# Kernel tuning notes

Measured on AMD Instinct MI355X. Metric: run time of the kernel, lower is better.

## Reference

```python
import jax, jax.numpy as jnp
import numpy as np
from jax import lax

N, IN_DIM, OUT_DIM, E, K = 100000, 128, 128, 600000, 3

def _xavier(key, shape):
    fan_out, fan_in = shape[0], shape[1]
    limit = float(np.sqrt(6.0 / (fan_in + fan_out)))
    return jax.random.uniform(key, shape, jnp.float32, -limit, limit)

def setup_inputs() -> dict:
    key = jax.random.key(0)
    ks = jax.random.split(key, 8)
    x = jax.random.normal(ks[0], (N, IN_DIM), jnp.float32)
    edge_index0 = jax.random.randint(ks[1], (2, E), 0, N, jnp.int64)
    edge_index1 = jax.random.randint(ks[2], (2, E), 0, N, jnp.int64)
    # relation Linear weights, torch layout [out_dim, in_dim]
    W_rel = jnp.stack([_xavier(ks[3], (OUT_DIM, IN_DIM)), _xavier(ks[4], (OUT_DIM, IN_DIM))])
    W_self = _xavier(ks[5], (OUT_DIM, IN_DIM))
    # Conv1d weight [out_ch, in_ch, k], bias [out_ch]
    fan = OUT_DIM * K
    conv_w = jax.random.uniform(ks[6], (OUT_DIM, OUT_DIM, K), jnp.float32, -1.0/np.sqrt(fan), 1.0/np.sqrt(fan))
    conv_b = jax.random.uniform(ks[7], (OUT_DIM,), jnp.float32, -1.0/np.sqrt(fan), 1.0/np.sqrt(fan))
    return {"x": x, "edge_index0": edge_index0, "edge_index1": edge_index1,
            "W_rel": W_rel, "W_self": W_self, "conv_w": conv_w, "conv_b": conv_b}

def reference(x, edge_index0, edge_index1, W_rel, W_self, conv_w, conv_b):
    num_nodes = x.shape[0]
    agg = jnp.zeros((num_nodes, W_rel.shape[1]), x.dtype)
    # per-relation: gather source feats -> linear -> scatter_add into target rows
    for ei, W in ((edge_index0, W_rel[0]), (edge_index1, W_rel[1])):
        src, tgt = ei[0], ei[1]
        messages = x[src] @ W.T                      # [E, out_dim]
        agg = agg.at[tgt].add(messages)
    # self loop
    agg = agg + x @ W_self.T
    # temporal Conv1d over node axis: [1, out_dim, N], kernel 3, padding 1, + ReLU
    # (Dropout is identity in eval mode)
    y = lax.conv_general_dilated(agg.T[None], conv_w, window_strides=(1,),
                                 padding=[(1, 1)],
                                 dimension_numbers=("NCH", "OIH", "NCH"))
    y = jax.nn.relu(y + conv_b[None, :, None])
    return y[0].T                                    # [N, out_dim]
```

## Files before the change

### kernel.cpp

```cpp
#include <hip/hip_runtime.h>
#include <hip/hip_bf16.h>

typedef __hip_bfloat16 bf16;
typedef short v8s __attribute__((ext_vector_type(8)));
typedef float v4f __attribute__((ext_vector_type(4)));
typedef unsigned int u32;

#define BFLO(u) __uint_as_float((u) << 16)
#define BFHI(u) __uint_as_float((u) & 0xffff0000u)

#define CH 4096
#define MAXNB 800

__device__ __forceinline__ int block_stride(const int* e0, int E, int* sm) {
    int t = threadIdx.x;
    if (t == 0) *sm = 0;
    __syncthreads();
    int nz = 0;
    for (int i = t; i < 2048; i += 256) {
        int slot = 2 * i + 1;
        if (slot < 2 * E) nz |= (e0[slot] != 0);
    }
    if (nz) atomicOr(sm, 1);
    __syncthreads();
    return *sm ? 1 : 2;
}


__global__ __launch_bounds__(256) void front_kernel(const float4* __restrict__ x4,
                                                    uint2* __restrict__ Ab,
                                                    const float* __restrict__ Wrel,
                                                    const float* __restrict__ Wself,
                                                    const float* __restrict__ convw,
                                                    const float* __restrict__ convb,
                                                    bf16* __restrict__ B1T,
                                                    bf16* __restrict__ B2T,
                                                    float* __restrict__ cbf,
                                                    const int* __restrict__ e0,
                                                    const int* __restrict__ e1,
                                                    int* __restrict__ gcnt,
                                                    int N, int E, int nbrr,
                                                    int cvtBlocks, int prepBlocks) {
    int b = blockIdx.x;
    if (b < cvtBlocks) {
        int i = b * 256 + threadIdx.x;
        if (i >= N * 32) return;
        int n = i >> 5, g = i & 31;
        float4 f = x4[i];
        union { uint2 u; bf16 h[4]; } o;
        o.h[0] = __float2bfloat16(f.x); o.h[1] = __float2bfloat16(f.y);
        o.h[2] = __float2bfloat16(f.z); o.h[3] = __float2bfloat16(f.w);
        Ab[(size_t)n * 96 + 64 + g] = o.u;
    } else if (b < cvtBlocks + prepBlocks) {
        int i = (b - cvtBlocks) * 256 + threadIdx.x;
        if (i < 49152) {
            int co = i / 384, k = i % 384;
            float v;
            if (k < 128)      v = Wrel[co * 128 + k];
            else if (k < 256) v = Wrel[16384 + co * 128 + (k - 128)];
            else              v = Wself[co * 128 + (k - 256)];
            B1T[i] = __float2bfloat16(v);
        } else if (i < 98304) {
            int j = i - 49152;
            int co = j / 384, k = j % 384, kk = k >> 7, ci = k & 127;
            B2T[j] = __float2bfloat16(convw[co * 384 + ci * 3 + kk]);
        } else if (i < 98432) {
            int c = i - 98304;
            cbf[c] = convb[c];
        }
    } else {
        __shared__ int hist[MAXNB];
        __shared__ int smf;
        int st = block_stride(e0, E, &smf);
        int NB = 2 * nbrr;
        int t = threadIdx.x;
        for (int i = t; i < NB; i += 256) hist[i] = 0;
        __syncthreads();
        long base = (long)(b - cvtBlocks - prepBlocks) * CH;
#pragma unroll
        for (int j = 0; j < CH / 256; ++j) {
            long e = base + j * 256 + t;
            if (e < 2 * (long)E) {
                int r = e >= E;
                long idx = r ? e - E : e;
                int tgt = (r ? e1 : e0)[(size_t)(E + idx) * st];
                atomicAdd(&hist[r * nbrr + (tgt >> 8)], 1);
            }
        }
        __syncthreads();
        for (int i = t; i < NB; i += 256) if (hist[i]) atomicAdd(&gcnt[i], hist[i]);
    }
}


__global__ __launch_bounds__(256) void bscan_kernel(const int* __restrict__ gcnt,
                                                    int* __restrict__ gbase,
                                                    int* __restrict__ gcur, int NB) {
    __shared__ int tsum[256];
    int t = threadIdx.x;
    int v[4]; int s = 0;
#pragma unroll
    for (int j = 0; j < 4; ++j) { int i = t * 4 + j; v[j] = (i < NB) ? gcnt[i] : 0; s += v[j]; }
    tsum[t] = s; __syncthreads();
    for (int d = 1; d < 256; d <<= 1) {
        int add = (t >= d) ? tsum[t - d] : 0;
        __syncthreads(); tsum[t] += add; __syncthreads();
    }
    int run = tsum[t] - s;
#pragma unroll
    for (int j = 0; j < 4; ++j) {
        int i = t * 4 + j;
        if (i < NB) { gbase[i] = run; gcur[i] = run; }
        run += v[j];
    }
    if (t == 255) gbase[NB] = run;
}


__global__ __launch_bounds__(256) void dist_kernel(const int* __restrict__ e0,
                                                   const int* __restrict__ e1,
                                                   int* __restrict__ gcur,
                                                   unsigned int* __restrict__ esorted,
                                                   int E, int nbrr) {
    __shared__ int hist[MAXNB], lstart[MAXNB], lcur[MAXNB], runbase[MAXNB];
    __shared__ unsigned int ordered[CH];
    __shared__ int tsum[256];
    __shared__ int smf;
    int st = block_stride(e0, E, &smf);
    int NB = 2 * nbrr;
    int t = threadIdx.x;
    for (int i = t; i < NB; i += 256) { hist[i] = 0; lcur[i] = 0; }
    __syncthreads();
    long base = (long)blockIdx.x * CH;
    unsigned int rec[CH / 256]; short bk[CH / 256];
#pragma unroll
    for (int j = 0; j < CH / 256; ++j) {
        long e = base + j * 256 + t;
        if (e < 2 * (long)E) {
            int r = e >= E;
            long idx = r ? e - E : e;
            const int* ei = r ? e1 : e0;
            int src = ei[(size_t)idx * st];
            int tgt = ei[(size_t)(E + idx) * st];
            bk[j] = (short)(r * nbrr + (tgt >> 8));
            rec[j] = (unsigned int)src | ((unsigned int)(tgt & 255) << 17);
            atomicAdd(&hist[bk[j]], 1);
        } else bk[j] = -1;
    }
    __syncthreads();
    {
        int vv[4]; int s = 0;
#pragma unroll
        for (int j = 0; j < 4; ++j) { int i = t * 4 + j; vv[j] = (i < NB) ? hist[i] : 0; s += vv[j]; }
        tsum[t] = s; __syncthreads();
        for (int d = 1; d < 256; d <<= 1) {
            int add = (t >= d) ? tsum[t - d] : 0;
            __syncthreads(); tsum[t] += add; __syncthreads();
        }
        int run = tsum[t] - s;
#pragma unroll
        for (int j = 0; j < 4; ++j) { int i = t * 4 + j; if (i < NB) { lstart[i] = run; run += vv[j]; } }
    }
    __syncthreads();
    for (int i = t; i < NB; i += 256) if (hist[i]) runbase[i] = atomicAdd(&gcur[i], hist[i]);
    __syncthreads();
#pragma unroll
    for (int j = 0; j < CH / 256; ++j) if (bk[j] >= 0) {
        int p = lstart[bk[j]] + atomicAdd(&lcur[bk[j]], 1);
        ordered[p] = rec[j];
    }
    __syncthreads();
    int w = t >> 6, lane = t & 63;
    for (int b = w; b < NB; b += 4) {
        int n = hist[b];
        if (n) {
            int gp = runbase[b], lp = lstart[b];
            for (int q = lane; q < n; q += 64) esorted[gp + q] = ordered[lp + q];
        }
    }
}


__global__ __launch_bounds__(256) void csr_kernel(const unsigned int* __restrict__ esorted,
                                                  const int* __restrict__ gbase,
                                                  int* __restrict__ off, int* __restrict__ cnt,
                                                  int* __restrict__ esrc, int N, int nbrr) {
    __shared__ int hist[256], lcur[256], tsum[256];
    int b = blockIdx.x;
    int r = b >= nbrr;
    int g = r ? b - nbrr : b;
    int t = threadIdx.x;
    int s0 = gbase[b], s1 = gbase[b + 1];
    hist[t] = 0;
    __syncthreads();
    for (int i = s0 + t; i < s1; i += 256)
        atomicAdd(&hist[(esorted[i] >> 17) & 255], 1);
    __syncthreads();
    int h = hist[t];
    tsum[t] = h; __syncthreads();
    for (int d = 1; d < 256; d <<= 1) {
        int add = (t >= d) ? tsum[t - d] : 0;
        __syncthreads(); tsum[t] += add; __syncthreads();
    }
    int start = tsum[t] - h;
    int node = g * 256 + t;
    if (node < N) { off[r * N + node] = s0 + start; cnt[r * N + node] = h; }
    lcur[t] = start;
    __syncthreads();
    for (int i = s0 + t; i < s1; i += 256) {
        unsigned int rec = esorted[i];
        int tl = (rec >> 17) & 255;
        int p = atomicAdd(&lcur[tl], 1);
        esrc[s0 + p] = rec & 0x1FFFF;
    }
}

__global__ __launch_bounds__(256) void gather_kernel(const int* __restrict__ off,
                                                     const int* __restrict__ cnt,
                                                     const int* __restrict__ esrc,
                                                     uint4* __restrict__ Ab4, int N) {
    int grp = blockIdx.x * 16 + (threadIdx.x >> 4);
    int lane = threadIdx.x & 15;
    if (grp >= 2 * N) return;
    int r = (grp >= N);
    int n = r ? grp - N : grp;
    int s0 = off[grp], c = cnt[grp];
    float a0 = 0.f, a1 = 0.f, a2 = 0.f, a3 = 0.f, a4 = 0.f, a5 = 0.f, a6 = 0.f, a7 = 0.f;
    for (int i0 = 0; i0 < c; i0 += 8) {
        int cm1 = c - 1;
        int s[8]; uint4 v[8];
#pragma unroll
        for (int u = 0; u < 8; ++u) {
            int j = i0 + u; j = (j <= cm1) ? j : cm1;
            s[u] = esrc[s0 + j];
        }
#pragma unroll
        for (int u = 0; u < 8; ++u)
            v[u] = Ab4[(size_t)s[u] * 48 + 32 + lane];
#pragma unroll
        for (int u = 0; u < 8; ++u) {
            if (i0 + u < c) {
                a0 += BFLO(v[u].x); a1 += BFHI(v[u].x);
                a2 += BFLO(v[u].y); a3 += BFHI(v[u].y);
                a4 += BFLO(v[u].z); a5 += BFHI(v[u].z);
                a6 += BFLO(v[u].w); a7 += BFHI(v[u].w);
            }
        }
    }
    union { uint4 u; bf16 h[8]; } o;
    o.h[0] = __float2bfloat16(a0); o.h[1] = __float2bfloat16(a1);
    o.h[2] = __float2bfloat16(a2); o.h[3] = __float2bfloat16(a3);
    o.h[4] = __float2bfloat16(a4); o.h[5] = __float2bfloat16(a5);
    o.h[6] = __float2bfloat16(a6); o.h[7] = __float2bfloat16(a7);
    Ab4[(size_t)n * 48 + (size_t)r * 16 + lane] = o.u;
}


__device__ __forceinline__ void gl2lds16(const void* g, void* l) {
    __builtin_amdgcn_global_load_lds(
        (const __attribute__((address_space(1))) u32*)g,
        (__attribute__((address_space(3))) u32*)l, 16, 0, 0);
}

__global__ __launch_bounds__(256) void gemm12_kernel(const bf16* __restrict__ Ab,
                                                     const bf16* __restrict__ B1T,
                                                     const bf16* __restrict__ B2T,
                                                     const float* __restrict__ cbf,
                                                     float* __restrict__ out, int M) {
    __shared__ __align__(16) char ldsbuf[52016];
    bf16* agg = (bf16*)ldsbuf;
    char* Ast = ldsbuf;
    char* Bst = ldsbuf + 35632;

    int t = threadIdx.x;
    int lane = t & 63, wv = t >> 6;
    int r = lane & 15, qq = lane >> 4;
    int m0 = blockIdx.x * 128;
    int swz = (r & 7) << 4;
    int lsw = ((lane & 7) ^ (lane >> 3)) << 4;

    int rowLo = (m0 < 8) ? 8 - m0 : 0;
    int rowHi = (m0 + 136 > M) ? M - m0 + 8 : 144;
    bool bdry = (rowLo > 0) || (rowHi < 144);

    const char* AbB = (const char*)Ab;
    const char* B1B = (const char*)B1T;
    const char* B2B = (const char*)B2T;

    v4f acc[9][2] = {};
    for (int kt = 0; kt < 6; ++kt) {
        int k0b = kt * 128;
        for (int c = wv; c < 34; c += 4) {
            if (c < 18) {
                int ar = m0 - 8 + c * 8 + (lane >> 3);
                ar = ar < 0 ? 0 : (ar >= M ? M - 1 : ar);
                gl2lds16(AbB + (size_t)ar * 768 + k0b + lsw, Ast + c * 1024);
            } else {
                int row = (c - 18) * 8 + (lane >> 3);
                gl2lds16(B1B + (size_t)row * 768 + k0b + lsw, Bst + (c - 18) * 1024);
            }
        }
        __syncthreads();
        if (bdry) {
            int* A4 = (int*)Ast;
            for (int i = t; i < rowLo * 32; i += 256) A4[i] = 0;
            for (int i = t; i < (144 - rowHi) * 32; i += 256) A4[rowHi * 32 + i] = 0;
            __syncthreads();
        }
#pragma unroll
        for (int ks = 0; ks < 2; ++ks) {
            int cb = (ks * 64 + qq * 16) ^ swz;
            v8s bfr[2];
#pragma unroll
            for (int tn = 0; tn < 2; ++tn)
                bfr[tn] = *(const v8s*)(Bst + (wv * 32 + tn * 16 + r) * 128 + cb);
#pragma unroll
            for (int tm = 0; tm < 9; ++tm) {
                v8s af = *(const v8s*)(Ast + (tm * 16 + r) * 128 + cb);
#pragma unroll
                for (int tn = 0; tn < 2; ++tn)
                    acc[tm][tn] = __builtin_amdgcn_mfma_f32_16x16x32_bf16(af, bfr[tn], acc[tm][tn], 0, 0, 0);
            }
        }
        __syncthreads();
    }
#pragma unroll
    for (int tm = 0; tm < 9; ++tm)
#pragma unroll
        for (int tn = 0; tn < 2; ++tn)
#pragma unroll
            for (int reg = 0; reg < 4; ++reg) {
                int row = tm * 16 + qq * 4 + reg;
                if (row >= 7 && row < 138)
                    agg[(row - 7) * 136 + wv * 32 + tn * 16 + r] =
                        __float2bfloat16(acc[tm][tn][reg]);
            }
    __syncthreads();

    v4f acc2[8][2] = {};
    for (int kt = 0; kt < 6; ++kt) {
        int k0b = kt * 128;
        int kk = kt >> 1;
        int rem = (kt & 1) * 64;
        for (int c = wv; c < 16; c += 4)
            gl2lds16(B2B + (size_t)(c * 8 + (lane >> 3)) * 768 + k0b + lsw, Bst + c * 1024);
        __syncthreads();
#pragma unroll
        for (int ks = 0; ks < 2; ++ks) {
            int cb = (ks * 64 + qq * 16) ^ swz;
            v8s bfr[2];
#pragma unroll
            for (int tn = 0; tn < 2; ++tn)
                bfr[tn] = *(const v8s*)(Bst + (wv * 32 + tn * 16 + r) * 128 + cb);
#pragma unroll
            for (int tm = 0; tm < 8; ++tm) {
                v8s af = *(const v8s*)&agg[(tm * 16 + r + kk) * 136 + rem + ks * 32 + qq * 8];
#pragma unroll
                for (int tn = 0; tn < 2; ++tn)
                    acc2[tm][tn] = __builtin_amdgcn_mfma_f32_16x16x32_bf16(af, bfr[tn], acc2[tm][tn], 0, 0, 0);
            }
        }
        __syncthreads();
    }
#pragma unroll
    for (int tm = 0; tm < 8; ++tm)
#pragma unroll
        for (int tn = 0; tn < 2; ++tn) {
            int col = wv * 32 + tn * 16 + r;
            float bias = cbf[col];
#pragma unroll
            for (int reg = 0; reg < 4; ++reg) {
                int grow = m0 + tm * 16 + qq * 4 + reg;
                if (grow < M) {
                    float v = acc2[tm][tn][reg] + bias;
                    out[(size_t)grow * 128 + col] = fmaxf(v, 0.f);
                }
            }
        }
}


extern "C" void kernel_launch(void* const* d_in, const int* in_sizes, int n_in,
                              void* d_out, int out_size, void* d_ws, size_t ws_size,
                              hipStream_t stream) {
    const float* x     = (const float*)d_in[0];
    const int*   e0    = (const int*)d_in[1];
    const int*   e1    = (const int*)d_in[2];
    const float* Wrel  = (const float*)d_in[3];
    const float* Wself = (const float*)d_in[4];
    const float* convw = (const float*)d_in[5];
    const float* convb = (const float*)d_in[6];
    float* out = (float*)d_out;

    int N = in_sizes[0] / 128;
    int E = in_sizes[1] / 2;
    int nbrr = (N + 255) >> 8;
    int NB = 2 * nbrr;

    char* p = (char*)d_ws;
    auto alloc = [&](size_t bytes) { char* q = p; p += (bytes + 255) & ~(size_t)255; return q; };
    int*  gcnt  = (int*)alloc((size_t)MAXNB * 4);
    int*  gbase = (int*)alloc((size_t)(MAXNB + 1) * 4);
    int*  gcur  = (int*)alloc((size_t)MAXNB * 4);
    unsigned int* esorted = (unsigned int*)alloc((size_t)2 * E * 4);
    int*  esrc  = (int*)alloc((size_t)2 * E * 4);
    int*  off   = (int*)alloc((size_t)2 * N * 4);
    int*  cnt   = (int*)alloc((size_t)2 * N * 4);
    bf16* Ab   = (bf16*)alloc((size_t)N * 384 * 2);
    bf16* B1T  = (bf16*)alloc(384 * 128 * 2);
    bf16* B2T  = (bf16*)alloc(384 * 128 * 2);
    float* cbf = (float*)alloc(512);

    hipMemsetAsync(gcnt, 0, (size_t)NB * 4, stream);

    int cvtBlocks = (N * 32 + 255) / 256;
    int prepBlocks = (98432 + 255) / 256;
    int chBlocks = (2 * E + CH - 1) / CH;
    front_kernel<<<cvtBlocks + prepBlocks + chBlocks, 256, 0, stream>>>(
        (const float4*)x, (uint2*)Ab, Wrel, Wself, convw, convb,
        B1T, B2T, cbf, e0, e1, gcnt, N, E, nbrr, cvtBlocks, prepBlocks);

    bscan_kernel<<<1, 256, 0, stream>>>(gcnt, gbase, gcur, NB);
    dist_kernel<<<chBlocks, 256, 0, stream>>>(e0, e1, gcur, esorted, E, nbrr);
    csr_kernel<<<NB, 256, 0, stream>>>(esorted, gbase, off, cnt, esrc, N, nbrr);

    gather_kernel<<<(2 * N + 15) / 16, 256, 0, stream>>>(off, cnt, esrc, (uint4*)Ab, N);

    int mBlocks = (N + 127) / 128;
    gemm12_kernel<<<mBlocks, 256, 0, stream>>>(Ab, B1T, B2T, cbf, out, N);
}
```

Before: 289.0 us.

## Double-buffer A tiles in fused GEMM, load B fragments directly to registers

```diff
diff --git a/kernel.cpp b/kernel.cpp
--- a/kernel.cpp
+++ b/kernel.cpp
@@ -262,15 +262,15 @@
         (__attribute__((address_space(3))) u32*)l, 16, 0, 0);
 }
 
-__global__ __launch_bounds__(256) void gemm12_kernel(const bf16* __restrict__ Ab,
-                                                     const bf16* __restrict__ B1T,
-                                                     const bf16* __restrict__ B2T,
-                                                     const float* __restrict__ cbf,
-                                                     float* __restrict__ out, int M) {
-    __shared__ __align__(16) char ldsbuf[52016];
+__global__ __launch_bounds__(256, 4) void gemm12_kernel(const bf16* __restrict__ Ab,
+                                                        const bf16* __restrict__ B1T,
+                                                        const bf16* __restrict__ B2T,
+                                                        const float* __restrict__ cbf,
+                                                        const float* __restrict__ zpad,
+                                                        float* __restrict__ out, int M) {
+    __shared__ __align__(16) char ldsbuf[36864];
     bf16* agg = (bf16*)ldsbuf;
     char* Ast = ldsbuf;
-    char* Bst = ldsbuf + 35632;
 
     int t = threadIdx.x;
     int lane = t & 63, wv = t >> 6;
@@ -279,51 +279,63 @@
     int swz = (r & 7) << 4;
     int lsw = ((lane & 7) ^ (lane >> 3)) << 4;
 
-    int rowLo = (m0 < 8) ? 8 - m0 : 0;
-    int rowHi = (m0 + 136 > M) ? M - m0 + 8 : 144;
-    bool bdry = (rowLo > 0) || (rowHi < 144);
-
     const char* AbB = (const char*)Ab;
     const char* B1B = (const char*)B1T;
     const char* B2B = (const char*)B2T;
-
+    const char* zB  = (const char*)zpad;
+
+    int c0 = (wv < 2) ? wv * 5 : 10 + (wv - 2) * 4;
+    int c1 = (wv < 2) ? c0 + 5 : c0 + 4;
+    size_t browB = (size_t)(wv * 32 + r) * 768;
+
+    auto STAGE = [&](int kt, int buf) {
+        int k0b = kt * 128;
+        char* dst = Ast + buf * 18432;
+        for (int c = c0; c < c1; ++c) {
+            int ar = m0 - 8 + c * 8 + (lane >> 3);
+            const char* src = (ar >= 0 && ar < M) ? (AbB + (size_t)ar * 768 + k0b + lsw)
+                                                  : (zB + lsw);
+            gl2lds16(src, dst + c * 1024);
+        }
+    };
+
+    STAGE(0, 0);
     v4f acc[9][2] = {};
     for (int kt = 0; kt < 6; ++kt) {
+        __builtin_amdgcn_s_barrier();
         int k0b = kt * 128;
-        for (int c = wv; c < 34; c += 4) {
-            if (c < 18) {
-                int ar = m0 - 8 + c * 8 + (lane >> 3);
-                ar = ar < 0 ? 0 : (ar >= M ? M - 1 : ar);
-                gl2lds16(AbB + (size_t)ar * 768 + k0b + lsw, Ast + c * 1024);
-            } else {
-                int row = (c - 18) * 8 + (lane >> 3);
-                gl2lds16(B1B + (size_t)row * 768 + k0b + lsw, Bst + (c - 18) * 1024);
-            }
-        }
-        __syncthreads();
-        if (bdry) {
-            int* A4 = (int*)Ast;
-            for (int i = t; i < rowLo * 32; i += 256) A4[i] = 0;
-            for (int i = t; i < (144 - rowHi) * 32; i += 256) A4[rowHi * 32 + i] = 0;
-            __syncthreads();
-        }
+        v8s bq[2][2];
+#pragma unroll
+        for (int ks = 0; ks < 2; ++ks)
+#pragma unroll
+            for (int tn = 0; tn < 2; ++tn)
+                bq[ks][tn] = *(const v8s*)(B1B + browB + (size_t)tn * 16 * 768 + k0b + ks * 64 + qq * 16);
+        __builtin_amdgcn_sched_barrier(0);
+        if (kt < 5) {
+            STAGE(kt + 1, (kt + 1) & 1);
+            if (wv < 2) asm volatile("s_waitcnt vmcnt(5)" ::: "memory");
+            else        asm volatile("s_waitcnt vmcnt(4)" ::: "memory");
+        } else {
+            asm volatile("s_waitcnt vmcnt(0)" ::: "memory");
+        }
+        __builtin_amdgcn_s_barrier();
+        __builtin_amdgcn_sched_barrier(0);
+        const char* Acur = Ast + (kt & 1) * 18432;
+        __builtin_amdgcn_s_setprio(1);
 #pragma unroll
         for (int ks = 0; ks < 2; ++ks) {
             int cb = (ks * 64 + qq * 16) ^ swz;
-            v8s bfr[2];
-#pragma unroll
-            for (int tn = 0; tn < 2; ++tn)
-                bfr[tn] = *(const v8s*)(Bst + (wv * 32 + tn * 16 + r) * 128 + cb);
 #pragma unroll
             for (int tm = 0; tm < 9; ++tm) {
-                v8s af = *(const v8s*)(Ast + (tm * 16 + r) * 128 + cb);
+                v8s af = *(const v8s*)(Acur + (tm * 16 + r) * 128 + cb);
 #pragma unroll
                 for (int tn = 0; tn < 2; ++tn)
-                    acc[tm][tn] = __builtin_amdgcn_mfma_f32_16x16x32_bf16(af, bfr[tn], acc[tm][tn], 0, 0, 0);
-            }
-        }
-        __syncthreads();
-    }
+                    acc[tm][tn] = __builtin_amdgcn_mfma_f32_16x16x32_bf16(af, bq[ks][tn], acc[tm][tn], 0, 0, 0);
+            }
+        }
+        __builtin_amdgcn_s_setprio(0);
+    }
+    __builtin_amdgcn_s_barrier();
 #pragma unroll
     for (int tm = 0; tm < 9; ++tm)
 #pragma unroll
@@ -332,35 +344,33 @@
             for (int reg = 0; reg < 4; ++reg) {
                 int row = tm * 16 + qq * 4 + reg;
                 if (row >= 7 && row < 138)
-                    agg[(row - 7) * 136 + wv * 32 + tn * 16 + r] =
+                    agg[(row - 7) * 140 + wv * 32 + tn * 16 + r] =
                         __float2bfloat16(acc[tm][tn][reg]);
             }
-    __syncthreads();
+    asm volatile("s_waitcnt lgkmcnt(0)" ::: "memory");
+    __builtin_amdgcn_s_barrier();
 
     v4f acc2[8][2] = {};
     for (int kt = 0; kt < 6; ++kt) {
         int k0b = kt * 128;
         int kk = kt >> 1;
         int rem = (kt & 1) * 64;
-        for (int c = wv; c < 16; c += 4)
-            gl2lds16(B2B + (size_t)(c * 8 + (lane >> 3)) * 768 + k0b + lsw, Bst + c * 1024);
-        __syncthreads();
+        v8s bq[2][2];
+#pragma unroll
+        for (int ks = 0; ks < 2; ++ks)
+#pragma unroll
+            for (int tn = 0; tn < 2; ++tn)
+                bq[ks][tn] = *(const v8s*)(B2B + browB + (size_t)tn * 16 * 768 + k0b + ks * 64 + qq * 16);
 #pragma unroll
         for (int ks = 0; ks < 2; ++ks) {
-            int cb = (ks * 64 + qq * 16) ^ swz;
-            v8s bfr[2];
-#pragma unroll
-            for (int tn = 0; tn < 2; ++tn)
-                bfr[tn] = *(const v8s*)(Bst + (wv * 32 + tn * 16 + r) * 128 + cb);
 #pragma unroll
             for (int tm = 0; tm < 8; ++tm) {
-                v8s af = *(const v8s*)&agg[(tm * 16 + r + kk) * 136 + rem + ks * 32 + qq * 8];
+                v8s af = *(const v8s*)&agg[(tm * 16 + r + kk) * 140 + rem + ks * 32 + qq * 8];
 #pragma unroll
                 for (int tn = 0; tn < 2; ++tn)
-                    acc2[tm][tn] = __builtin_amdgcn_mfma_f32_16x16x32_bf16(af, bfr[tn], acc2[tm][tn], 0, 0, 0);
-            }
-        }
-        __syncthreads();
+                    acc2[tm][tn] = __builtin_amdgcn_mfma_f32_16x16x32_bf16(af, bq[ks][tn], acc2[tm][tn], 0, 0, 0);
+            }
+        }
     }
 #pragma unroll
     for (int tm = 0; tm < 8; ++tm)
@@ -410,8 +420,10 @@
     bf16* B1T  = (bf16*)alloc(384 * 128 * 2);
     bf16* B2T  = (bf16*)alloc(384 * 128 * 2);
     float* cbf = (float*)alloc(512);
+    float* zpad = (float*)alloc(256);
 
     hipMemsetAsync(gcnt, 0, (size_t)NB * 4, stream);
+    hipMemsetAsync(zpad, 0, 256, stream);
 
     int cvtBlocks = (N * 32 + 255) / 256;
     int prepBlocks = (98432 + 255) / 256;
@@ -427,5 +439,5 @@
     gather_kernel<<<(2 * N + 15) / 16, 256, 0, stream>>>(off, cnt, esrc, (uint4*)Ab, N);
 
     int mBlocks = (N + 127) / 128;
-    gemm12_kernel<<<mBlocks, 256, 0, stream>>>(Ab, B1T, B2T, cbf, out, N);
-}
+    gemm12_kernel<<<mBlocks, 256, 0, stream>>>(Ab, B1T, B2T, cbf, zpad, out, N);
+}
```

Result: slower. 310.9 us (+7.6%).

## Double-buffer LDS loads in fused GEMM and shrink row tile to fit

Applied to the files above, without the earlier changes.

```diff
diff --git a/kernel.cpp b/kernel.cpp
--- a/kernel.cpp
+++ b/kernel.cpp
@@ -267,103 +267,131 @@
                                                      const bf16* __restrict__ B2T,
                                                      const float* __restrict__ cbf,
                                                      float* __restrict__ out, int M) {
-    __shared__ __align__(16) char ldsbuf[52016];
+    __shared__ __align__(16) char ldsbuf[65536];
     bf16* agg = (bf16*)ldsbuf;
-    char* Ast = ldsbuf;
-    char* Bst = ldsbuf + 35632;
 
     int t = threadIdx.x;
     int lane = t & 63, wv = t >> 6;
     int r = lane & 15, qq = lane >> 4;
-    int m0 = blockIdx.x * 128;
+    int m0 = blockIdx.x * 112;
     int swz = (r & 7) << 4;
     int lsw = ((lane & 7) ^ (lane >> 3)) << 4;
 
     int rowLo = (m0 < 8) ? 8 - m0 : 0;
-    int rowHi = (m0 + 136 > M) ? M - m0 + 8 : 144;
-    bool bdry = (rowLo > 0) || (rowHi < 144);
+    int rowHi = (m0 + 120 > M) ? M - m0 + 8 : 128;
+    bool bdry = (rowLo > 0) || (rowHi < 128);
 
     const char* AbB = (const char*)Ab;
     const char* B1B = (const char*)B1T;
     const char* B2B = (const char*)B2T;
 
-    v4f acc[9][2] = {};
-    for (int kt = 0; kt < 6; ++kt) {
+    auto STAGE1 = [&](int kt) {
         int k0b = kt * 128;
-        for (int c = wv; c < 34; c += 4) {
-            if (c < 18) {
+        char* dst = ldsbuf + (kt & 1) * 32768;
+        for (int c = wv; c < 32; c += 4) {
+            if (c < 16) {
                 int ar = m0 - 8 + c * 8 + (lane >> 3);
                 ar = ar < 0 ? 0 : (ar >= M ? M - 1 : ar);
-                gl2lds16(AbB + (size_t)ar * 768 + k0b + lsw, Ast + c * 1024);
+                gl2lds16(AbB + (size_t)ar * 768 + k0b + lsw, dst + c * 1024);
             } else {
-                int row = (c - 18) * 8 + (lane >> 3);
-                gl2lds16(B1B + (size_t)row * 768 + k0b + lsw, Bst + (c - 18) * 1024);
-            }
-        }
-        __syncthreads();
+                int row = (c - 16) * 8 + (lane >> 3);
+                gl2lds16(B1B + (size_t)row * 768 + k0b + lsw, dst + 16384 + (c - 16) * 1024);
+            }
+        }
+    };
+    auto STAGE2 = [&](int kt) {
+        int k0b = kt * 128;
+        char* dst = ldsbuf + 32768 + (kt & 1) * 16384;
+        for (int c = wv; c < 16; c += 4) {
+            int row = c * 8 + (lane >> 3);
+            gl2lds16(B2B + (size_t)row * 768 + k0b + lsw, dst + c * 1024);
+        }
+    };
+
+    STAGE1(0);
+    v4f acc[8][2] = {};
+    for (int kt = 0; kt < 6; ++kt) {
+        if (kt > 0) __builtin_amdgcn_s_barrier();
+        if (kt < 5) STAGE1(kt + 1);
+        __builtin_amdgcn_sched_barrier(0);
+        if (kt < 5) asm volatile("s_waitcnt vmcnt(8)" ::: "memory");
+        else        asm volatile("s_waitcnt vmcnt(0)" ::: "memory");
+        __builtin_amdgcn_sched_barrier(0);
+        __builtin_amdgcn_s_barrier();
+        const char* Ac = ldsbuf + (kt & 1) * 32768;
         if (bdry) {
-            int* A4 = (int*)Ast;
+            int* A4 = (int*)Ac;
             for (int i = t; i < rowLo * 32; i += 256) A4[i] = 0;
-            for (int i = t; i < (144 - rowHi) * 32; i += 256) A4[rowHi * 32 + i] = 0;
+            for (int i = t; i < (128 - rowHi) * 32; i += 256) A4[rowHi * 32 + i] = 0;
             __syncthreads();
         }
+        __builtin_amdgcn_s_setprio(1);
 #pragma unroll
         for (int ks = 0; ks < 2; ++ks) {
             int cb = (ks * 64 + qq * 16) ^ swz;
             v8s bfr[2];
 #pragma unroll
             for (int tn = 0; tn < 2; ++tn)
-                bfr[tn] = *(const v8s*)(Bst + (wv * 32 + tn * 16 + r) * 128 + cb);
-#pragma unroll
-            for (int tm = 0; tm < 9; ++tm) {
-                v8s af = *(const v8s*)(Ast + (tm * 16 + r) * 128 + cb);
+                bfr[tn] = *(const v8s*)(Ac + 16384 + (wv * 32 + tn * 16 + r) * 128 + cb);
+#pragma unroll
+            for (int tm = 0; tm < 8; ++tm) {
+                v8s af = *(const v8s*)(Ac + (tm * 16 + r) * 128 + cb);
 #pragma unroll
                 for (int tn = 0; tn < 2; ++tn)
                     acc[tm][tn] = __builtin_amdgcn_mfma_f32_16x16x32_bf16(af, bfr[tn], acc[tm][tn], 0, 0, 0);
             }
         }
-        __syncthreads();
-    }
-#pragma unroll
-    for (int tm = 0; tm < 9; ++tm)
+        __builtin_amdgcn_s_setprio(0);
+    }
+    __builtin_amdgcn_s_barrier();
+
+    STAGE2(0);
+#pragma unroll
+    for (int tm = 0; tm < 8; ++tm)
 #pragma unroll
         for (int tn = 0; tn < 2; ++tn)
 #pragma unroll
             for (int reg = 0; reg < 4; ++reg) {
                 int row = tm * 16 + qq * 4 + reg;
-                if (row >= 7 && row < 138)
+                if (row >= 7 && row < 121)
                     agg[(row - 7) * 136 + wv * 32 + tn * 16 + r] =
                         __float2bfloat16(acc[tm][tn][reg]);
             }
-    __syncthreads();
-
-    v4f acc2[8][2] = {};
+    asm volatile("s_waitcnt lgkmcnt(0)" ::: "memory");
+    __builtin_amdgcn_s_barrier();
+
+    v4f acc2[7][2] = {};
     for (int kt = 0; kt < 6; ++kt) {
-        int k0b = kt * 128;
+        if (kt > 0) __builtin_amdgcn_s_barrier();
+        if (kt < 5) STAGE2(kt + 1);
+        __builtin_amdgcn_sched_barrier(0);
+        if (kt < 5) asm volatile("s_waitcnt vmcnt(4)" ::: "memory");
+        else        asm volatile("s_waitcnt vmcnt(0)" ::: "memory");
+        __builtin_amdgcn_sched_barrier(0);
+        __builtin_amdgcn_s_barrier();
+        const char* Bc = ldsbuf + 32768 + (kt & 1) * 16384;
         int kk = kt >> 1;
         int rem = (kt & 1) * 64;
-        for (int c = wv; c < 16; c += 4)
-            gl2lds16(B2B + (size_t)(c * 8 + (lane >> 3)) * 768 + k0b + lsw, Bst + c * 1024);
-        __syncthreads();
+        __builtin_amdgcn_s_setprio(1);
 #pragma unroll
         for (int ks = 0; ks < 2; ++ks) {
             int cb = (ks * 64 + qq * 16) ^ swz;
             v8s bfr[2];
 #pragma unroll
             for (int tn = 0; tn < 2; ++tn)
-                bfr[tn] = *(const v8s*)(Bst + (wv * 32 + tn * 16 + r) * 128 + cb);
-#pragma unroll
-            for (int tm = 0; tm < 8; ++tm) {
+                bfr[tn] = *(const v8s*)(Bc + (wv * 32 + tn * 16 + r) * 128 + cb);
+#pragma unroll
+            for (int tm = 0; tm < 7; ++tm) {
                 v8s af = *(const v8s*)&agg[(tm * 16 + r + kk) * 136 + rem + ks * 32 + qq * 8];
 #pragma unroll
                 for (int tn = 0; tn < 2; ++tn)
                     acc2[tm][tn] = __builtin_amdgcn_mfma_f32_16x16x32_bf16(af, bfr[tn], acc2[tm][tn], 0, 0, 0);
             }
         }
-        __syncthreads();
-    }
-#pragma unroll
-    for (int tm = 0; tm < 8; ++tm)
+        __builtin_amdgcn_s_setprio(0);
+    }
+#pragma unroll
+    for (int tm = 0; tm < 7; ++tm)
 #pragma unroll
         for (int tn = 0; tn < 2; ++tn) {
             int col = wv * 32 + tn * 16 + r;
@@ -426,6 +454,6 @@
 
     gather_kernel<<<(2 * N + 15) / 16, 256, 0, stream>>>(off, cnt, esrc, (uint4*)Ab, N);
 
-    int mBlocks = (N + 127) / 128;
+    int mBlocks = (N + 111) / 112;
     gemm12_kernel<<<mBlocks, 256, 0, stream>>>(Ab, B1T, B2T, cbf, out, N);
 }
```

Result: no change. 284.8 us (-1.5%).
